# Kernel tuning notes

Hardware: AMD Instinct MI355X
Metric: run time of the kernel (lower is better)

The kernel has to match this reference:

```python
import jax, jax.numpy as jnp
import numpy as np
import math

EPS = 1e-8
H, DM, S = 16, 1024, 128  # heads, d_model, seq_len (== channels)
DK = DM // H


def _fq_act_uint8(x):
    # Brevitas Uint8ActPerTensorFloat: per-tensor unsigned 8-bit fake-quant (negatives clip to 0)
    s = jnp.maximum(jnp.max(x), EPS) / 255.0
    return jnp.clip(jnp.round(x / s), 0.0, 255.0) * s


def _fq_w_int8(w):
    # Int8 weight per-tensor, narrow range [-127, 127]
    s = jnp.maximum(jnp.max(jnp.abs(w)), EPS) / 127.0
    return jnp.clip(jnp.round(w / s), -127.0, 127.0) * s, s


def _fq_pc_int8(x, axis):
    # QuantIdentity: signed 8-bit fake-quant, per-channel scale along `axis` (abs-max stats)
    red = tuple(i for i in range(x.ndim) if i != axis)
    s = jnp.maximum(jnp.max(jnp.abs(x), axis=red, keepdims=True), EPS) / 127.0
    return jnp.clip(jnp.round(x / s), -128.0, 127.0) * s


def _quant_linear(x, W, b):
    # QuantLinear: uint8 input quant, int8 weight quant, Int32 bias quant (scale = s_in * s_w)
    s_in = jnp.maximum(jnp.max(x), EPS) / 255.0
    xq = jnp.clip(jnp.round(x / s_in), 0.0, 255.0) * s_in
    Wq, s_w = _fq_w_int8(W)
    s_b = s_in * s_w
    bq = jnp.round(b / s_b) * s_b
    return jnp.einsum('bsd,od->bso', xq, Wq) + bq


def setup_inputs() -> dict:
    key = jax.random.key(0)
    ks = jax.random.split(key, 12)
    B = 64
    std = 1.0 / math.sqrt(DM)
    inp = {
        'query': jax.random.normal(ks[0], (B, S, DM), jnp.float32),
        'key':   jax.random.normal(ks[1], (B, S, DM), jnp.float32),
        'value': jax.random.normal(ks[2], (B, S, DM), jnp.float32),
        'mask':  jnp.ones((B, S, S), jnp.int32),
    }
    for i, nm in enumerate(['q', 'k', 'v', 'o']):
        inp[f'W{nm}'] = jax.random.normal(ks[3 + i], (DM, DM), jnp.float32) * std
        inp[f'b{nm}'] = jax.random.normal(ks[7 + i], (DM,), jnp.float32) * 0.01
    return inp


def reference(query, key, value, mask, Wq, bq, Wk, bk, Wv, bv, Wo, bo):
    B = query.shape[0]
    # QuantLinear projections -> [B, h, S, d_k]
    def proj(x, W, b):
        return _quant_linear(x, W, b).reshape(B, S, H, DK).transpose(0, 2, 1, 3)
    q = proj(query, Wq, bq)
    k = proj(key, Wk, bk)
    v = proj(value, Wv, bv)

    # quantizer_1: per-channel on q rows (axis 2); quantizer_2: on k^T columns (axis 3)
    kt = jnp.swapaxes(k, -2, -1)  # [B, h, d_k, S]
    scores = jnp.matmul(_fq_pc_int8(q, 2), _fq_pc_int8(kt, 3)) / math.sqrt(DK)
    scores = jnp.where(mask[:, None, :, :] == 0, -1e9, scores)
    p_attn = jax.nn.softmax(scores, axis=-1)

    # quantizer_3: per-channel on p_attn columns (axis 3); quantizer_4: on v rows (axis 2)
    x = jnp.matmul(_fq_pc_int8(p_attn, 3), _fq_pc_int8(v, 2))  # [B, h, S, d_k]
    x = x.transpose(0, 2, 1, 3).reshape(B, S, DM)
    return _quant_linear(x, Wo, bo)
```

## Files before the change

### kernel.cpp

```cpp
#include <hip/hip_runtime.h>
#include <hip/hip_bf16.h>
#include <math.h>

typedef unsigned short u16;
typedef unsigned int u32;
typedef unsigned long long u64;
typedef signed char i8;

constexpr int NB = 64, NS = 128, NDM = 1024, NH = 16, NDK = 64;
constexpr int NM = NB * NS;
constexpr float QEPS = 1e-8f;

typedef __attribute__((ext_vector_type(8))) short short8;
typedef __attribute__((ext_vector_type(4))) float f32x4;
typedef __attribute__((ext_vector_type(4))) int i32x4;

__device__ __forceinline__ u32 fenc(float f) {
  u32 u = __float_as_uint(f);
  return (u & 0x80000000u) ? ~u : (u | 0x80000000u);
}
__device__ __forceinline__ float fdec(u32 u) {
  u = (u & 0x80000000u) ? (u & 0x7FFFFFFFu) : ~u;
  return __uint_as_float(u);
}
__device__ __forceinline__ u16 f2bf(float f) { return (u16)(__float_as_uint(f) >> 16); }
__device__ __forceinline__ float bf2f(u16 u) { return __uint_as_float(((u32)u) << 16); }

__device__ __forceinline__ void glds16(const void* g, void* l) {
  __builtin_amdgcn_global_load_lds(
      (const __attribute__((address_space(1))) void*)(unsigned long long)(uintptr_t)g,
      (__attribute__((address_space(3))) void*)(u32)(uintptr_t)l, 16, 0, 0);
}


__global__ void init_kernel(u32* scl) {
  for (int i = threadIdx.x; i < 2048; i += blockDim.x) scl[i] = 0u;
}

__global__ void maskbits_kernel(const int* __restrict__ mask, u64* __restrict__ mb) {
  int row = blockIdx.x * 4 + (threadIdx.x >> 6);
  int lane = threadIdx.x & 63;
  const int* mrow = mask + (size_t)row * NS;
  u64 b0 = __ballot(mrow[lane] != 0);
  u64 b1 = __ballot(mrow[64 + lane] != 0);
  if (lane == 0) { mb[row * 2] = b0; mb[row * 2 + 1] = b1; }
}

__global__ void fused_max_kernel(const float* __restrict__ q, const float* __restrict__ k,
                                 const float* __restrict__ v, const float* __restrict__ w0,
                                 const float* __restrict__ w1, const float* __restrict__ w2,
                                 const float* __restrict__ w3, u32* __restrict__ sclu) {
  int y = blockIdx.y;
  const float* src; size_t n4; int ab;
  switch (y) {
    case 0: src = q; n4 = (size_t)NM * NDM / 4; ab = 0; break;
    case 1: src = k; n4 = (size_t)NM * NDM / 4; ab = 0; break;
    case 2: src = v; n4 = (size_t)NM * NDM / 4; ab = 0; break;
    case 3: src = w0; n4 = (size_t)NDM * NDM / 4; ab = 1; break;
    case 4: src = w1; n4 = (size_t)NDM * NDM / 4; ab = 1; break;
    case 5: src = w2; n4 = (size_t)NDM * NDM / 4; ab = 1; break;
    default: src = w3; n4 = (size_t)NDM * NDM / 4; ab = 1; break;
  }
  float m = -INFINITY;
  size_t stride = (size_t)gridDim.x * blockDim.x;
  for (size_t i = (size_t)blockIdx.x * blockDim.x + threadIdx.x; i < n4; i += stride) {
    float4 f = ((const float4*)src)[i];
    if (ab) { f.x = fabsf(f.x); f.y = fabsf(f.y); f.z = fabsf(f.z); f.w = fabsf(f.w); }
    m = fmaxf(m, fmaxf(fmaxf(f.x, f.y), fmaxf(f.z, f.w)));
  }
  for (int off = 32; off; off >>= 1) m = fmaxf(m, __shfl_down(m, off));
  __shared__ float sm[4];
  if ((threadIdx.x & 63) == 0) sm[threadIdx.x >> 6] = m;
  __syncthreads();
  if (threadIdx.x == 0) {
    float r = fmaxf(fmaxf(sm[0], sm[1]), fmaxf(sm[2], sm[3]));
    atomicMax(&sclu[y], fenc(r));
  }
}

__global__ void quant_w_kernel(const float* __restrict__ w0, const float* __restrict__ w1,
                               const float* __restrict__ w2, const float* __restrict__ w3,
                               u16* __restrict__ dst, const u32* __restrict__ sclu) {
  int y = blockIdx.y;
  const float* src = y == 0 ? w0 : y == 1 ? w1 : y == 2 ? w2 : w3;
  u16* d = dst + (size_t)y * NDM * NDM;
  float s = fmaxf(fdec(sclu[3 + y]), QEPS) / 127.0f;
  size_t n4 = (size_t)NDM * NDM / 4;
  size_t stride = (size_t)gridDim.x * blockDim.x;
  for (size_t i = (size_t)blockIdx.x * blockDim.x + threadIdx.x; i < n4; i += stride) {
    float4 f = ((const float4*)src)[i];
    ushort4 o;
    o.x = f2bf(fminf(fmaxf(rintf(f.x / s), -127.f), 127.f));
    o.y = f2bf(fminf(fmaxf(rintf(f.y / s), -127.f), 127.f));
    o.z = f2bf(fminf(fmaxf(rintf(f.z / s), -127.f), 127.f));
    o.w = f2bf(fminf(fmaxf(rintf(f.w / s), -127.f), 127.f));
    ((ushort4*)d)[i] = o;
  }
}

__global__ void quant_u8_kernel(const float* __restrict__ src, u16* __restrict__ dst,
                                const u32* __restrict__ slot) {
  float s = fmaxf(fdec(*slot), QEPS) / 255.0f;
  size_t n4 = (size_t)NM * NDM / 4;
  size_t stride = (size_t)gridDim.x * blockDim.x;
  for (size_t i = (size_t)blockIdx.x * blockDim.x + threadIdx.x; i < n4; i += stride) {
    float4 f = ((const float4*)src)[i];
    ushort4 o;
    o.x = f2bf(fminf(fmaxf(rintf(f.x / s), 0.f), 255.f));
    o.y = f2bf(fminf(fmaxf(rintf(f.y / s), 0.f), 255.f));
    o.z = f2bf(fminf(fmaxf(rintf(f.z / s), 0.f), 255.f));
    o.w = f2bf(fminf(fmaxf(rintf(f.w / s), 0.f), 255.f));
    ((ushort4*)dst)[i] = o;
  }
}

__global__ void qkv_i8_kernel(const float* __restrict__ projbase, i8* __restrict__ dstbase,
                              const float* __restrict__ scl) {
  int y = blockIdx.y;
  const float* src = projbase + (size_t)y * NM * NDM;
  i8* dst = dstbase + (size_t)y * NM * NDM;
  const float* sb = scl + 8 + y * 128;
  size_t n4 = (size_t)NM * NDM / 4;
  size_t stride = (size_t)gridDim.x * blockDim.x;
  for (size_t i = (size_t)blockIdx.x * blockDim.x + threadIdx.x; i < n4; i += stride) {
    int s_idx = (int)((i >> 8) & 127);
    float s = fmaxf(sb[s_idx], QEPS) / 127.0f;
    float4 f = ((const float4*)src)[i];
    int a = (int)fminf(fmaxf(rintf(f.x / s), -128.f), 127.f);
    int b = (int)fminf(fmaxf(rintf(f.y / s), -128.f), 127.f);
    int c = (int)fminf(fmaxf(rintf(f.z / s), -128.f), 127.f);
    int d = (int)fminf(fmaxf(rintf(f.w / s), -128.f), 127.f);
    ((int*)dst)[i] = (a & 255) | ((b & 255) << 8) | ((c & 255) << 16) | ((d & 255) << 24);
  }
}

constexpr int BM = 128, BN = 128, BK = 32;

template <bool PROJ>
__global__ __launch_bounds__(256)
void gemm_kernel(const u16* __restrict__ Abase, const u16* __restrict__ Wbase,
                 const float* __restrict__ b0, const float* __restrict__ b1,
                 const float* __restrict__ b2, float* __restrict__ Cbase,
                 u32* __restrict__ sclu) {
  constexpr int K = NDM, N = NDM;
  const int z = PROJ ? blockIdx.z : 0;
  const u16* A = Abase + (size_t)z * NM * NDM;
  const u16* Wt = PROJ ? (Wbase + (size_t)z * NDM * NDM) : Wbase;
  const float* bias = PROJ ? (z == 0 ? b0 : z == 1 ? b1 : b2) : b0;
  float* C = PROJ ? (Cbase + (size_t)z * NM * NDM) : Cbase;
  const u32* slot_in = PROJ ? (sclu + z) : (sclu + 7);
  const u32* slot_w = PROJ ? (sclu + 3 + z) : (sclu + 6);

  __shared__ __align__(16) u16 As[BM][BK];
  __shared__ __align__(16) u16 Bs[BN][BK];
  __shared__ float rmax2[2][BM];

  const int tid = threadIdx.x;
  const int lane = tid & 63, wave = tid >> 6;
  const int wm = (wave & 1) * 64, wn = (wave >> 1) * 64;
  const int r16 = lane & 15, quad = lane >> 4;
  const int bm = blockIdx.x * BM, bn = blockIdx.y * BN;

  f32x4 acc[4][4] = {};

  const int lrow = lane >> 2, lcol = (lane & 3) * 8;
  for (int k0 = 0; k0 < K; k0 += BK) {
    __syncthreads();
#pragma unroll
    for (int p = 0; p < 2; p++) {
      int r = wave * 32 + p * 16;
      glds16(A + (size_t)(bm + r + lrow) * K + k0 + lcol, &As[r][0]);
      glds16(Wt + (size_t)(bn + r + lrow) * K + k0 + lcol, &Bs[r][0]);
    }
    __syncthreads();
    short8 af[4], bfr[4];
#pragma unroll
    for (int i = 0; i < 4; i++) af[i] = *(const short8*)(&As[wm + i * 16 + r16][quad * 8]);
#pragma unroll
    for (int j = 0; j < 4; j++) bfr[j] = *(const short8*)(&Bs[wn + j * 16 + r16][quad * 8]);
#pragma unroll
    for (int i = 0; i < 4; i++)
#pragma unroll
      for (int j = 0; j < 4; j++)
        acc[i][j] = __builtin_amdgcn_mfma_f32_16x16x32_bf16(af[i], bfr[j], acc[i][j], 0, 0, 0);
  }

  float s_in = fmaxf(fdec(*slot_in), QEPS) / 255.0f;
  float s_w = fmaxf(fdec(*slot_w), QEPS) / 127.0f;
  float sc = s_in * s_w;

  float bq[4];
#pragma unroll
  for (int j = 0; j < 4; j++) {
    int gc = bn + wn + j * 16 + r16;
    bq[j] = rintf(bias[gc] / sc) * sc;
  }
#pragma unroll
  for (int i = 0; i < 4; i++) {
#pragma unroll
    for (int r = 0; r < 4; r++) {
      int lr = wm + i * 16 + quad * 4 + r;
      int gr = bm + lr;
      float rm = 0.0f;
#pragma unroll
      for (int j = 0; j < 4; j++) {
        int gc = bn + wn + j * 16 + r16;
        float val = acc[i][j][r] * sc + bq[j];
        C[(size_t)gr * N + gc] = val;
        if (PROJ) rm = fmaxf(rm, fabsf(val));
      }
      if (PROJ) {
#pragma unroll
        for (int off = 1; off < 16; off <<= 1) rm = fmaxf(rm, __shfl_xor(rm, off));
        if (r16 == 0) rmax2[wave >> 1][lr] = rm;
      }
    }
  }
  if (PROJ) {
    __syncthreads();
    if (tid < BM) {
      float m = fmaxf(rmax2[0][tid], rmax2[1][tid]);
      atomicMax((int*)&sclu[8 + z * 128 + tid], __float_as_int(m));
    }
  }
}

__global__ __launch_bounds__(256)
void attn_scores_kernel(const i8* __restrict__ qi8, const i8* __restrict__ ki8,
                        const u64* __restrict__ mb, const float* __restrict__ scl,
                        u32* __restrict__ sclu, float* __restrict__ Pn) {
  const int bh = blockIdx.x, b = bh >> 4, h = bh & 15;
  const int tid = threadIdx.x, lane = tid & 63, wave = tid >> 6;
  const int r16 = lane & 15, quad = lane >> 4;

  __shared__ __align__(16) i8 Qs[NS][80];
  __shared__ __align__(16) i8 Ks[NS][80];
  __shared__ float sqv[NS], skv[NS];
  __shared__ float cmw[4][NS];

  {
    int row = tid >> 1, half = (tid & 1) * 32;
    const i8* qp = qi8 + (size_t)(b * NS + row) * NDM + h * NDK + half;
    const i8* kp = ki8 + (size_t)(b * NS + row) * NDM + h * NDK + half;
    *(int4*)&Qs[row][half] = *(const int4*)qp;
    *(int4*)&Qs[row][half + 16] = *(const int4*)(qp + 16);
    *(int4*)&Ks[row][half] = *(const int4*)kp;
    *(int4*)&Ks[row][half + 16] = *(const int4*)(kp + 16);
    if (tid < NS) {
      sqv[tid] = fmaxf(scl[8 + tid], QEPS) / 127.0f;
      skv[tid] = fmaxf(scl[8 + 128 + tid], QEPS) / 127.0f;
    }
  }
  __syncthreads();

  const int rowbase = wave * 32;
  i32x4 acc[2][8] = {};
#pragma unroll
  for (int mt = 0; mt < 2; mt++) {
    i32x4 a = *(const i32x4*)&Qs[rowbase + mt * 16 + r16][quad * 16];
#pragma unroll
    for (int nt = 0; nt < 8; nt++) {
      i32x4 bfrag = *(const i32x4*)&Ks[nt * 16 + r16][quad * 16];
      acc[mt][nt] = __builtin_amdgcn_mfma_i32_16x16x64_i8(a, bfrag, acc[mt][nt], 0, 0, 0);
    }
  }

  float skc[8], cm[8];
#pragma unroll
  for (int nt = 0; nt < 8; nt++) { skc[nt] = skv[nt * 16 + r16]; cm[nt] = 0.0f; }

#pragma unroll
  for (int mt = 0; mt < 2; mt++) {
#pragma unroll
    for (int r = 0; r < 4; r++) {
      int row = rowbase + mt * 16 + quad * 4 + r;
      float sq = sqv[row];
      const u64* mrow = mb + ((size_t)b * NS + row) * 2;
      u64 m0 = mrow[0], m1 = mrow[1];
      float vals[8];
      float mx = -INFINITY;
#pragma unroll
      for (int nt = 0; nt < 8; nt++) {
        float v = (float)acc[mt][nt][r] * (sq * skc[nt]) * 0.125f;
        u64 bits = nt < 4 ? m0 : m1;
        if (((bits >> ((nt * 16 + r16) & 63)) & 1ull) == 0) v = -1e9f;
        vals[nt] = v;
        mx = fmaxf(mx, v);
      }
#pragma unroll
      for (int off = 1; off < 16; off <<= 1) mx = fmaxf(mx, __shfl_xor(mx, off));
      float sum = 0.0f;
#pragma unroll
      for (int nt = 0; nt < 8; nt++) { vals[nt] = __expf(vals[nt] - mx); sum += vals[nt]; }
#pragma unroll
      for (int off = 1; off < 16; off <<= 1) sum += __shfl_xor(sum, off);
      float* prow = Pn + ((size_t)bh * NS + row) * NS;
#pragma unroll
      for (int nt = 0; nt < 8; nt++) {
        float p = vals[nt] / sum;
        prow[nt * 16 + r16] = p;
        cm[nt] = fmaxf(cm[nt], p);
      }
    }
  }

#pragma unroll
  for (int nt = 0; nt < 8; nt++) {
    float c = cm[nt];
    c = fmaxf(c, __shfl_xor(c, 16));
    c = fmaxf(c, __shfl_xor(c, 32));
    if (quad == 0) cmw[wave][nt * 16 + r16] = c;
  }
  __syncthreads();
  if (tid < NS) {
    float c = fmaxf(fmaxf(cmw[0][tid], cmw[1][tid]), fmaxf(cmw[2][tid], cmw[3][tid]));
    atomicMax((int*)&sclu[392 + tid], __float_as_int(c));
  }
}

__global__ __launch_bounds__(256)
void attn_pv_kernel(const float* __restrict__ Pn, const i8* __restrict__ vi8,
                    const float* __restrict__ scl, float* __restrict__ xout,
                    u32* __restrict__ xmax_slot) {
  const int bh = blockIdx.x, b = bh >> 4, h = bh & 15;
  const int tid = threadIdx.x, lane = tid & 63, wave = tid >> 6;
  const int r16 = lane & 15, quad = lane >> 4;
  const int rowbase = wave * 32;

  __shared__ __align__(16) u16 Ps[NS][72];
  __shared__ __align__(16) u16 Vhi[64][72];
  __shared__ __align__(16) u16 Vlo[64][72];
  __shared__ float spv[NS], svv[NS];

  if (tid < NS) {
    spv[tid] = fmaxf(scl[392 + tid], QEPS) / 127.0f;
    svv[tid] = fmaxf(scl[8 + 256 + tid], QEPS) / 127.0f;
  }

  f32x4 xacc[2][4] = {};
  for (int half = 0; half < 2; half++) {
    __syncthreads();
    {
      int row = tid >> 1, jl0 = (tid & 1) * 32;
      const float* prow = Pn + ((size_t)bh * NS + row) * NS + half * 64 + jl0;
#pragma unroll
      for (int c4 = 0; c4 < 8; c4++) {
        float4 p = *(const float4*)(prow + c4 * 4);
        int j = half * 64 + jl0 + c4 * 4;
        ushort4 o;
        o.x = f2bf(fminf(fmaxf(rintf(p.x / spv[j + 0]), -128.f), 127.f));
        o.y = f2bf(fminf(fmaxf(rintf(p.y / spv[j + 1]), -128.f), 127.f));
        o.z = f2bf(fminf(fmaxf(rintf(p.z / spv[j + 2]), -128.f), 127.f));
        o.w = f2bf(fminf(fmaxf(rintf(p.w / spv[j + 3]), -128.f), 127.f));
        *(ushort4*)&Ps[row][jl0 + c4 * 4] = o;
      }
    }
    {
      int jl = tid >> 2, d0 = (tid & 3) * 16;
      int j = half * 64 + jl;
      float g = spv[j] * svv[j];
      const i8* vp = vi8 + (size_t)(b * NS + j) * NDM + h * NDK + d0;
      int4 raw = *(const int4*)vp;
      const i8* rb = (const i8*)&raw;
#pragma unroll
      for (int d = 0; d < 16; d++) {
        float w = (float)rb[d] * g;
        u16 hi = f2bf(w);
        Vhi[d0 + d][jl] = hi;
        Vlo[d0 + d][jl] = f2bf(w - bf2f(hi));
      }
    }
    __syncthreads();
#pragma unroll
    for (int kk = 0; kk < 2; kk++) {
      short8 pa[2];
#pragma unroll
      for (int mt = 0; mt < 2; mt++)
        pa[mt] = *(const short8*)&Ps[rowbase + mt * 16 + r16][kk * 32 + quad * 8];
#pragma unroll
      for (int nt = 0; nt < 4; nt++) {
        short8 vh = *(const short8*)&Vhi[nt * 16 + r16][kk * 32 + quad * 8];
        short8 vl = *(const short8*)&Vlo[nt * 16 + r16][kk * 32 + quad * 8];
#pragma unroll
        for (int mt = 0; mt < 2; mt++) {
          xacc[mt][nt] = __builtin_amdgcn_mfma_f32_16x16x32_bf16(pa[mt], vh, xacc[mt][nt], 0, 0, 0);
          xacc[mt][nt] = __builtin_amdgcn_mfma_f32_16x16x32_bf16(pa[mt], vl, xacc[mt][nt], 0, 0, 0);
        }
      }
    }
  }

  float mx = -INFINITY;
#pragma unroll
  for (int mt = 0; mt < 2; mt++)
#pragma unroll
    for (int nt = 0; nt < 4; nt++)
#pragma unroll
      for (int r = 0; r < 4; r++) {
        int row = rowbase + mt * 16 + quad * 4 + r;
        xout[((size_t)b * NS + row) * NDM + h * NDK + nt * 16 + r16] = xacc[mt][nt][r];
        mx = fmaxf(mx, xacc[mt][nt][r]);
      }
#pragma unroll
  for (int off = 1; off < 64; off <<= 1) mx = fmaxf(mx, __shfl_xor(mx, off));
  if (lane == 0) atomicMax(xmax_slot, fenc(mx));
}

constexpr size_t OFF_SCL = 0;
constexpr size_t OFF_MB  = 8192;
constexpr size_t OFF_W   = OFF_MB + (size_t)NM * 16;
constexpr size_t OFF_XQ  = OFF_W + 4 * (size_t)NDM * NDM * 2;
constexpr size_t OFF_PQ  = OFF_XQ + 3 * (size_t)NM * NDM * 2;
constexpr size_t OFF_I8  = OFF_PQ + 3 * (size_t)NM * NDM * 4;

extern "C" void kernel_launch(void* const* d_in, const int* in_sizes, int n_in,
                              void* d_out, int out_size, void* d_ws, size_t ws_size,
                              hipStream_t stream) {
  const float* query = (const float*)d_in[0];
  const float* key = (const float*)d_in[1];
  const float* value = (const float*)d_in[2];
  const int* mask = (const int*)d_in[3];
  const float* Wq = (const float*)d_in[4]; const float* bq = (const float*)d_in[5];
  const float* Wk = (const float*)d_in[6]; const float* bk = (const float*)d_in[7];
  const float* Wv = (const float*)d_in[8]; const float* bv = (const float*)d_in[9];
  const float* Wo = (const float*)d_in[10]; const float* bo = (const float*)d_in[11];

  char* ws = (char*)d_ws;
  float* scl = (float*)(ws + OFF_SCL);
  u32* sclu = (u32*)scl;
  u64* mb = (u64*)(ws + OFF_MB);
  u16* wb = (u16*)(ws + OFF_W);
  u16* wob = wb + 3 * (size_t)NDM * NDM;
  u16* xq = (u16*)(ws + OFF_XQ);
  float* proj = (float*)(ws + OFF_PQ);
  i8* qkv8 = (i8*)(ws + OFF_I8);
  float* Pn = proj;
  float* xout = proj + 2 * (size_t)NM * NDM;
  i8* vi8 = qkv8 + 2 * (size_t)NM * NDM;

  init_kernel<<<1, 256, 0, stream>>>(sclu);
  maskbits_kernel<<<NM / 4, 256, 0, stream>>>(mask, mb);
  fused_max_kernel<<<dim3(512, 7), 256, 0, stream>>>(query, key, value, Wq, Wk, Wv, Wo, sclu);
  quant_w_kernel<<<dim3(512, 4), 256, 0, stream>>>(Wq, Wk, Wv, Wo, wb, sclu);

  quant_u8_kernel<<<512, 256, 0, stream>>>(query, xq, sclu + 0);
  quant_u8_kernel<<<512, 256, 0, stream>>>(key, xq + (size_t)NM * NDM, sclu + 1);
  quant_u8_kernel<<<512, 256, 0, stream>>>(value, xq + 2 * (size_t)NM * NDM, sclu + 2);

  gemm_kernel<true><<<dim3(NM / BM, NDM / BN, 3), 256, 0, stream>>>(
      xq, wb, bq, bk, bv, proj, sclu);

  qkv_i8_kernel<<<dim3(512, 3), 256, 0, stream>>>(proj, qkv8, scl);

  attn_scores_kernel<<<NB * NH, 256, 0, stream>>>(qkv8, qkv8 + (size_t)NM * NDM, mb, scl,
                                                  sclu, Pn);
  attn_pv_kernel<<<NB * NH, 256, 0, stream>>>(Pn, vi8, scl, xout, sclu + 7);

  quant_u8_kernel<<<512, 256, 0, stream>>>(xout, xq, sclu + 7);
  gemm_kernel<false><<<dim3(NM / BM, NDM / BN, 1), 256, 0, stream>>>(
      xq, wob, bo, bo, bo, (float*)d_out, sclu);
}
```

Before: 474.8 us.

## Switch projection GEMMs to int8 MFMA with zero-point column-sum correction

Quantized activations and weights are now stored as int8 rather than bf16. Activations are shifted by -128 so uint8 values fit in signed int8, and a per-output-row weight sum times 128 is added back in the epilogue. The GEMMs use the i32 16x16x64 int8 MFMA with BK doubled to 64, which halves operand bytes and raises matrix throughput. The three activation quant launches are also merged into one kernel. Integer accumulation is exact, so this is a numerically equivalent change, though it relies on the int8 MFMA fragment layout being correct.

```diff
diff --git a/kernel.cpp b/kernel.cpp
--- a/kernel.cpp
+++ b/kernel.cpp
@@ -78,39 +78,45 @@
   }
 }
 
-__global__ void quant_w_kernel(const float* __restrict__ w0, const float* __restrict__ w1,
-                               const float* __restrict__ w2, const float* __restrict__ w3,
-                               u16* __restrict__ dst, const u32* __restrict__ sclu) {
+__global__ __launch_bounds__(256)
+void quant_w_i8_kernel(const float* __restrict__ w0, const float* __restrict__ w1,
+                       const float* __restrict__ w2, const float* __restrict__ w3,
+                       i8* __restrict__ dst, int* __restrict__ colsum,
+                       const u32* __restrict__ sclu) {
+  int y = blockIdx.y, row = blockIdx.x, tid = threadIdx.x;
+  const float* src = (y == 0 ? w0 : y == 1 ? w1 : y == 2 ? w2 : w3) + (size_t)row * NDM;
+  float s = fmaxf(fdec(sclu[3 + y]), QEPS) / 127.0f;
+  float4 f = ((const float4*)src)[tid];
+  int a = (int)fminf(fmaxf(rintf(f.x / s), -127.f), 127.f);
+  int b = (int)fminf(fmaxf(rintf(f.y / s), -127.f), 127.f);
+  int c = (int)fminf(fmaxf(rintf(f.z / s), -127.f), 127.f);
+  int d = (int)fminf(fmaxf(rintf(f.w / s), -127.f), 127.f);
+  ((int*)(dst + (size_t)y * NDM * NDM + (size_t)row * NDM))[tid] =
+      (a & 255) | ((b & 255) << 8) | ((c & 255) << 16) | ((d & 255) << 24);
+  int ssum = a + b + c + d;
+  for (int off = 32; off; off >>= 1) ssum += __shfl_down(ssum, off);
+  __shared__ int sm[4];
+  if ((tid & 63) == 0) sm[tid >> 6] = ssum;
+  __syncthreads();
+  if (tid == 0) colsum[y * NDM + row] = sm[0] + sm[1] + sm[2] + sm[3];
+}
+
+__global__ void quant_a_kernel(const float* __restrict__ s0, const float* __restrict__ s1,
+                               const float* __restrict__ s2, i8* __restrict__ dst,
+                               const u32* __restrict__ sclu, int slot_base) {
   int y = blockIdx.y;
-  const float* src = y == 0 ? w0 : y == 1 ? w1 : y == 2 ? w2 : w3;
-  u16* d = dst + (size_t)y * NDM * NDM;
-  float s = fmaxf(fdec(sclu[3 + y]), QEPS) / 127.0f;
-  size_t n4 = (size_t)NDM * NDM / 4;
-  size_t stride = (size_t)gridDim.x * blockDim.x;
-  for (size_t i = (size_t)blockIdx.x * blockDim.x + threadIdx.x; i < n4; i += stride) {
-    float4 f = ((const float4*)src)[i];
-    ushort4 o;
-    o.x = f2bf(fminf(fmaxf(rintf(f.x / s), -127.f), 127.f));
-    o.y = f2bf(fminf(fmaxf(rintf(f.y / s), -127.f), 127.f));
-    o.z = f2bf(fminf(fmaxf(rintf(f.z / s), -127.f), 127.f));
-    o.w = f2bf(fminf(fmaxf(rintf(f.w / s), -127.f), 127.f));
-    ((ushort4*)d)[i] = o;
-  }
-}
-
-__global__ void quant_u8_kernel(const float* __restrict__ src, u16* __restrict__ dst,
-                                const u32* __restrict__ slot) {
-  float s = fmaxf(fdec(*slot), QEPS) / 255.0f;
+  const float* src = y == 0 ? s0 : y == 1 ? s1 : s2;
+  i8* d = dst + (size_t)y * NM * NDM;
+  float s = fmaxf(fdec(sclu[slot_base + y]), QEPS) / 255.0f;
   size_t n4 = (size_t)NM * NDM / 4;
   size_t stride = (size_t)gridDim.x * blockDim.x;
   for (size_t i = (size_t)blockIdx.x * blockDim.x + threadIdx.x; i < n4; i += stride) {
     float4 f = ((const float4*)src)[i];
-    ushort4 o;
-    o.x = f2bf(fminf(fmaxf(rintf(f.x / s), 0.f), 255.f));
-    o.y = f2bf(fminf(fmaxf(rintf(f.y / s), 0.f), 255.f));
-    o.z = f2bf(fminf(fmaxf(rintf(f.z / s), 0.f), 255.f));
-    o.w = f2bf(fminf(fmaxf(rintf(f.w / s), 0.f), 255.f));
-    ((ushort4*)dst)[i] = o;
+    int a = (int)fminf(fmaxf(rintf(f.x / s), 0.f), 255.f) - 128;
+    int b = (int)fminf(fmaxf(rintf(f.y / s), 0.f), 255.f) - 128;
+    int c = (int)fminf(fmaxf(rintf(f.z / s), 0.f), 255.f) - 128;
+    int e = (int)fminf(fmaxf(rintf(f.w / s), 0.f), 255.f) - 128;
+    ((int*)d)[i] = (a & 255) | ((b & 255) << 8) | ((c & 255) << 16) | ((e & 255) << 24);
   }
 }
 
@@ -134,25 +140,26 @@
   }
 }
 
-constexpr int BM = 128, BN = 128, BK = 32;
+constexpr int BM = 128, BN = 128, BK = 64;
 
 template <bool PROJ>
 __global__ __launch_bounds__(256)
-void gemm_kernel(const u16* __restrict__ Abase, const u16* __restrict__ Wbase,
-                 const float* __restrict__ b0, const float* __restrict__ b1,
-                 const float* __restrict__ b2, float* __restrict__ Cbase,
-                 u32* __restrict__ sclu) {
+void gemm_kernel(const i8* __restrict__ Abase, const i8* __restrict__ Wbase,
+                 const int* __restrict__ colsum, const float* __restrict__ b0,
+                 const float* __restrict__ b1, const float* __restrict__ b2,
+                 float* __restrict__ Cbase, u32* __restrict__ sclu) {
   constexpr int K = NDM, N = NDM;
   const int z = PROJ ? blockIdx.z : 0;
-  const u16* A = Abase + (size_t)z * NM * NDM;
-  const u16* Wt = PROJ ? (Wbase + (size_t)z * NDM * NDM) : Wbase;
+  const i8* A = Abase + (size_t)z * NM * NDM;
+  const i8* Wt = PROJ ? (Wbase + (size_t)z * NDM * NDM) : Wbase;
   const float* bias = PROJ ? (z == 0 ? b0 : z == 1 ? b1 : b2) : b0;
   float* C = PROJ ? (Cbase + (size_t)z * NM * NDM) : Cbase;
   const u32* slot_in = PROJ ? (sclu + z) : (sclu + 7);
   const u32* slot_w = PROJ ? (sclu + 3 + z) : (sclu + 6);
-
-  __shared__ __align__(16) u16 As[BM][BK];
-  __shared__ __align__(16) u16 Bs[BN][BK];
+  const int* cs = colsum + (PROJ ? z : 3) * NDM;
+
+  __shared__ __align__(16) i8 As[BM][BK];
+  __shared__ __align__(16) i8 Bs[BN][BK];
   __shared__ float rmax2[2][BM];
 
   const int tid = threadIdx.x;
@@ -161,9 +168,9 @@
   const int r16 = lane & 15, quad = lane >> 4;
   const int bm = blockIdx.x * BM, bn = blockIdx.y * BN;
 
-  f32x4 acc[4][4] = {};
-
-  const int lrow = lane >> 2, lcol = (lane & 3) * 8;
+  i32x4 acc[4][4] = {};
+
+  const int lrow = lane >> 2, lcol = (lane & 3) * 16;
   for (int k0 = 0; k0 < K; k0 += BK) {
     __syncthreads();
 #pragma unroll
@@ -173,16 +180,16 @@
       glds16(Wt + (size_t)(bn + r + lrow) * K + k0 + lcol, &Bs[r][0]);
     }
     __syncthreads();
-    short8 af[4], bfr[4];
-#pragma unroll
-    for (int i = 0; i < 4; i++) af[i] = *(const short8*)(&As[wm + i * 16 + r16][quad * 8]);
-#pragma unroll
-    for (int j = 0; j < 4; j++) bfr[j] = *(const short8*)(&Bs[wn + j * 16 + r16][quad * 8]);
+    i32x4 af[4], bfr[4];
+#pragma unroll
+    for (int i = 0; i < 4; i++) af[i] = *(const i32x4*)(&As[wm + i * 16 + r16][quad * 16]);
+#pragma unroll
+    for (int j = 0; j < 4; j++) bfr[j] = *(const i32x4*)(&Bs[wn + j * 16 + r16][quad * 16]);
 #pragma unroll
     for (int i = 0; i < 4; i++)
 #pragma unroll
       for (int j = 0; j < 4; j++)
-        acc[i][j] = __builtin_amdgcn_mfma_f32_16x16x32_bf16(af[i], bfr[j], acc[i][j], 0, 0, 0);
+        acc[i][j] = __builtin_amdgcn_mfma_i32_16x16x64_i8(af[i], bfr[j], acc[i][j], 0, 0, 0);
   }
 
   float s_in = fmaxf(fdec(*slot_in), QEPS) / 255.0f;
@@ -190,10 +197,12 @@
   float sc = s_in * s_w;
 
   float bq[4];
+  int csj[4];
 #pragma unroll
   for (int j = 0; j < 4; j++) {
     int gc = bn + wn + j * 16 + r16;
     bq[j] = rintf(bias[gc] / sc) * sc;
+    csj[j] = cs[gc] << 7;
   }
 #pragma unroll
   for (int i = 0; i < 4; i++) {
@@ -205,7 +214,7 @@
 #pragma unroll
       for (int j = 0; j < 4; j++) {
         int gc = bn + wn + j * 16 + r16;
-        float val = acc[i][j][r] * sc + bq[j];
+        float val = (float)(acc[i][j][r] + csj[j]) * sc + bq[j];
         C[(size_t)gr * N + gc] = val;
         if (PROJ) rm = fmaxf(rm, fabsf(val));
       }
@@ -407,10 +416,11 @@
 }
 
 constexpr size_t OFF_SCL = 0;
-constexpr size_t OFF_MB  = 8192;
+constexpr size_t OFF_CS  = 8192;
+constexpr size_t OFF_MB  = OFF_CS + 4 * NDM * 4;
 constexpr size_t OFF_W   = OFF_MB + (size_t)NM * 16;
-constexpr size_t OFF_XQ  = OFF_W + 4 * (size_t)NDM * NDM * 2;
-constexpr size_t OFF_PQ  = OFF_XQ + 3 * (size_t)NM * NDM * 2;
+constexpr size_t OFF_XQ  = OFF_W + 4 * (size_t)NDM * NDM;
+constexpr size_t OFF_PQ  = OFF_XQ + 3 * (size_t)NM * NDM;
 constexpr size_t OFF_I8  = OFF_PQ + 3 * (size_t)NM * NDM * 4;
 
 extern "C" void kernel_launch(void* const* d_in, const int* in_sizes, int n_in,
@@ -428,10 +438,11 @@
   char* ws = (char*)d_ws;
   float* scl = (float*)(ws + OFF_SCL);
   u32* sclu = (u32*)scl;
+  int* colsum = (int*)(ws + OFF_CS);
   u64* mb = (u64*)(ws + OFF_MB);
-  u16* wb = (u16*)(ws + OFF_W);
-  u16* wob = wb + 3 * (size_t)NDM * NDM;
-  u16* xq = (u16*)(ws + OFF_XQ);
+  i8* wb = (i8*)(ws + OFF_W);
+  i8* wob = wb + 3 * (size_t)NDM * NDM;
+  i8* xq = (i8*)(ws + OFF_XQ);
   float* proj = (float*)(ws + OFF_PQ);
   i8* qkv8 = (i8*)(ws + OFF_I8);
   float* Pn = proj;
@@ -441,14 +452,11 @@
   init_kernel<<<1, 256, 0, stream>>>(sclu);
   maskbits_kernel<<<NM / 4, 256, 0, stream>>>(mask, mb);
   fused_max_kernel<<<dim3(512, 7), 256, 0, stream>>>(query, key, value, Wq, Wk, Wv, Wo, sclu);
-  quant_w_kernel<<<dim3(512, 4), 256, 0, stream>>>(Wq, Wk, Wv, Wo, wb, sclu);
-
-  quant_u8_kernel<<<512, 256, 0, stream>>>(query, xq, sclu + 0);
-  quant_u8_kernel<<<512, 256, 0, stream>>>(key, xq + (size_t)NM * NDM, sclu + 1);
-  quant_u8_kernel<<<512, 256, 0, stream>>>(value, xq + 2 * (size_t)NM * NDM, sclu + 2);
+  quant_w_i8_kernel<<<dim3(NDM, 4), 256, 0, stream>>>(Wq, Wk, Wv, Wo, wb, colsum, sclu);
+  quant_a_kernel<<<dim3(512, 3), 256, 0, stream>>>(query, key, value, xq, sclu, 0);
 
   gemm_kernel<true><<<dim3(NM / BM, NDM / BN, 3), 256, 0, stream>>>(
-      xq, wb, bq, bk, bv, proj, sclu);
+      xq, wb, colsum, bq, bk, bv, proj, sclu);
 
   qkv_i8_kernel<<<dim3(512, 3), 256, 0, stream>>>(proj, qkv8, scl);
 
@@ -456,7 +464,7 @@
                                                   sclu, Pn);
   attn_pv_kernel<<<NB * NH, 256, 0, stream>>>(Pn, vi8, scl, xout, sclu + 7);
 
-  quant_u8_kernel<<<512, 256, 0, stream>>>(xout, xq, sclu + 7);
+  quant_a_kernel<<<dim3(512, 1), 256, 0, stream>>>(xout, xout, xout, xq, sclu, 7);
   gemm_kernel<false><<<dim3(NM / BM, NDM / BN, 1), 256, 0, stream>>>(
-      xq, wob, bo, bo, bo, (float*)d_out, sclu);
-}
+      xq, wob, colsum, bo, bo, bo, (float*)d_out, sclu);
+}
```

Result: faster. 431.3 us (-9.2%).
